# Kernel tuning notes

Hardware: AMD Instinct MI355X
Metric: run time of the kernel (lower is better)

## Reference

```python
import jax, jax.numpy as jnp
import numpy as np

NUM_HEADS = 16
ROPE_THETA = 10000.0


def _rope_cos_sin(seq_len, head_dim, dtype):
    # theta_i = theta^(-2i/d_k), i in [0, d_k/2)
    i = jnp.arange(head_dim // 2, dtype=jnp.float32)
    inv_freq = ROPE_THETA ** (-2.0 * i / head_dim)
    pos = jnp.arange(seq_len, dtype=jnp.float32)[:, None]
    ang = pos * inv_freq[None, :]                      # [S, d/2]
    return jnp.cos(ang).astype(dtype), jnp.sin(ang).astype(dtype)


def _apply_rope(t, cos, sin):
    # t: [B, H, S, d]; rotate consecutive pairs (complex multiply)
    B, H, S, d = t.shape
    tp = t.reshape(B, H, S, d // 2, 2)
    x0, x1 = tp[..., 0], tp[..., 1]
    r0 = x0 * cos - x1 * sin
    r1 = x0 * sin + x1 * cos
    return jnp.stack([r0, r1], axis=-1).reshape(B, H, S, d)


def setup_inputs() -> dict:
    key = jax.random.key(0)
    k1, k2, k3 = jax.random.split(key, 3)
    B, S, D = 4, 2048, 1024
    x = jax.random.normal(k1, (B, S, D), dtype=jnp.float32)
    padding_mask = jnp.ones((B, S), dtype=jnp.int32)
    # trunc-normal-ish init, std = sqrt(2/(in+out))
    std_qkv = np.sqrt(2.0 / (D + 3 * D))
    w_qkv = jax.random.normal(k2, (3 * D, D), dtype=jnp.float32) * std_qkv
    w_o = jax.random.normal(k3, (D, D), dtype=jnp.float32) * 0.02
    return {"x": x, "padding_mask": padding_mask, "w_qkv": w_qkv, "w_o": w_o}


def reference(x, padding_mask, w_qkv, w_o):
    B, S, D = x.shape
    H = NUM_HEADS
    hd = D // H
    scale = 1.0 / np.sqrt(hd)

    qkv = x @ w_qkv.T                                   # [B, S, 3D]
    q, k, v = jnp.split(qkv, 3, axis=-1)

    def to_heads(t):
        return t.reshape(B, S, H, hd).transpose(0, 2, 1, 3)  # [B, H, S, hd]

    q, k, v = to_heads(q), to_heads(k), to_heads(v)

    cos, sin = _rope_cos_sin(S, hd, x.dtype)            # [S, hd/2]
    q = _apply_rope(q, cos, sin)
    k = _apply_rope(k, cos, sin)

    scores = jnp.einsum("bhqd,bhkd->bhqk", q, k) * scale  # [B, H, S, S]

    causal = jnp.tril(jnp.ones((S, S), dtype=x.dtype))
    mask = causal[None, :, :] * padding_mask.astype(x.dtype)[:, None, :]  # [B, S, S]
    scores = jnp.where(mask[:, None, :, :] == 0, -jnp.inf, scores)

    weights = jax.nn.softmax(scores, axis=-1)
    out = jnp.einsum("bhqk,bhkd->bhqd", weights, v)     # [B, H, S, hd]
    out = out.transpose(0, 2, 1, 3).reshape(B, S, D)
    return out @ w_o.T
```

## Files before the change

kernel.cpp:

```cpp
#include <hip/hip_runtime.h>

typedef unsigned short u16;
typedef unsigned int u32;
typedef __bf16 bf16x8 __attribute__((ext_vector_type(8)));
typedef float f32x4 __attribute__((ext_vector_type(4)));

#define MFMA_BF16(a, b, c) __builtin_amdgcn_mfma_f32_16x16x32_bf16((a), (b), (c), 0, 0, 0)

#define QSCALE 0.18033688011112042f
#define M0SHIFT 24.0f


__device__ __forceinline__ u16 f2bf(float f) {
  u32 u = __builtin_bit_cast(u32, f);
  u += 0x7fffu + ((u >> 16) & 1u);
  return (u16)(u >> 16);
}

__device__ __forceinline__ void async_copy16(const void* g, void* l) {
  __builtin_amdgcn_global_load_lds(
      (__attribute__((address_space(1))) void*)g,
      (__attribute__((address_space(3))) void*)l, 16, 0, 0);
}


__global__ __launch_bounds__(256) void prep_kernel(
    const float* __restrict__ x_f, const float* __restrict__ wqkv_f,
    const float* __restrict__ wo_f, u16* __restrict__ xb,
    u16* __restrict__ wqkvb, u16* __restrict__ wob, float2* __restrict__ rope_t) {
  const int blk = blockIdx.x;
  if (blk < 12288) {
    const float* src;
    u16* dst;
    int base;
    float scale = 1.0f;
    if (blk < 8192)      { src = x_f;    dst = xb;    base = blk; }
    else if (blk < 11264){ src = wqkv_f; dst = wqkvb; base = blk - 8192;
                           if (base < 1024) scale = QSCALE; }
    else                 { src = wo_f;   dst = wob;   base = blk - 11264; }
    const int i = base * 1024 + threadIdx.x * 4;
    const float4 v = *(const float4*)(src + i);
    ushort4 o;
    o.x = f2bf(v.x * scale); o.y = f2bf(v.y * scale);
    o.z = f2bf(v.z * scale); o.w = f2bf(v.w * scale);
    *(ushort4*)(dst + i) = o;
  } else {
    const int idx = (blk - 12288) * 256 + threadIdx.x;
    const int s = idx >> 5, i = idx & 31;
    const float invf = __builtin_amdgcn_exp2f(-(float)i * 0.41524101186092027f);
    float rev = (float)s * invf * 0.15915494309189535f;
    rev -= floorf(rev);
    rope_t[idx] = make_float2(__builtin_amdgcn_cosf(rev), __builtin_amdgcn_sinf(rev));
  }
}


__device__ __forceinline__ void gemm_bt_tile(const u16* A, const u16* B, int K,
                                             int row0, int col0,
                                             u16* lds, f32x4 acc[4][4]) {
  const int tid = threadIdx.x;
  const int wave = tid >> 6;
  const int lane = tid & 63;
  const int fr = lane & 15;
  const int quad = lane >> 4;
  const int wm = (wave >> 1) * 64;
  const int wn = (wave & 1) * 64;
  u16* a_lds = lds;
  u16* b_lds = lds + 4096;

  f32x4 zero = {0.f, 0.f, 0.f, 0.f};
#pragma unroll
  for (int mt = 0; mt < 4; ++mt)
#pragma unroll
    for (int nt = 0; nt < 4; ++nt) acc[mt][nt] = zero;

  for (int k0 = 0; k0 < K; k0 += 32) {
    __syncthreads();
#pragma unroll
    for (int c = 0; c < 2; ++c) {
      const int ebase = wave * 1024 + c * 512;
      const int e = ebase + lane * 8;
      const int r = e >> 5;
      const int kk = e & 31;
      async_copy16(A + (size_t)(row0 + r) * K + k0 + kk, a_lds + ebase);
      async_copy16(B + (size_t)(col0 + r) * K + k0 + kk, b_lds + ebase);
    }
    __syncthreads();

    bf16x8 a_frag[4], b_frag[4];
#pragma unroll
    for (int t = 0; t < 4; ++t) {
      a_frag[t] = *(const bf16x8*)(a_lds + (wm + t * 16 + fr) * 32 + quad * 8);
      b_frag[t] = *(const bf16x8*)(b_lds + (wn + t * 16 + fr) * 32 + quad * 8);
    }
#pragma unroll
    for (int mt = 0; mt < 4; ++mt)
#pragma unroll
      for (int nt = 0; nt < 4; ++nt)
        acc[mt][nt] = MFMA_BF16(a_frag[mt], b_frag[nt], acc[mt][nt]);
  }
}


__global__ __launch_bounds__(256) void qkv_rope_kernel(
    const u16* __restrict__ x, const u16* __restrict__ w_qkv,
    const float2* __restrict__ rope_t,
    u16* __restrict__ q_ws, u16* __restrict__ k_ws, u16* __restrict__ vt_ws) {
  __shared__ u16 sbuf[128 * 136];
  f32x4 acc[4][4];
  const int row0 = blockIdx.y * 128;
  const int col0 = blockIdx.x * 128;
  gemm_bt_tile(x, w_qkv, 1024, row0, col0, sbuf, acc);

  const int tid = threadIdx.x;
  const int wave = tid >> 6, lane = tid & 63;
  const int fr = lane & 15, quad = lane >> 4;
  const int wm = (wave >> 1) * 64, wn = (wave & 1) * 64;
  const int region = col0 >> 10;
  const int f0 = col0 & 1023;
  const int s0r = row0 & 2047;
  const int bb = row0 >> 11;

  __syncthreads();

  if (region < 2) {
#pragma unroll
    for (int mt = 0; mt < 4; ++mt) {
#pragma unroll
      for (int nt = 0; nt < 4; ++nt) {
        const int n = wn + nt * 16 + fr;
        const int d = n & 63;
#pragma unroll
        for (int r = 0; r < 4; ++r) {
          const int m = wm + mt * 16 + quad * 4 + r;
          const float own = acc[mt][nt][r];
          const float part = __shfl_xor(own, 1);
          const int s = s0r + m;
          const float2 cssn = rope_t[s * 32 + (d >> 1)];
          const float val = (d & 1) ? (part * cssn.y + own * cssn.x)
                                    : (own * cssn.x - part * cssn.y);
          sbuf[m * 136 + n] = f2bf(val);
        }
      }
    }
    __syncthreads();
    u16* dst = (region == 0) ? q_ws : k_ws;
    const int h0 = f0 >> 6;
#pragma unroll
    for (int j = 0; j < 8; ++j) {
      const int idx2 = j * 256 + tid;
      const int hf = idx2 >> 10;
      const int m = (idx2 & 1023) >> 3;
      const int c8 = (idx2 & 7) * 8;
      const uint4 v = *(const uint4*)(sbuf + m * 136 + hf * 64 + c8);
      *(uint4*)(dst + ((size_t)(bb * 16 + h0 + hf) * 2048 + s0r + m) * 64 + c8) = v;
    }
  } else {
#pragma unroll
    for (int mt = 0; mt < 4; ++mt)
#pragma unroll
      for (int nt = 0; nt < 4; ++nt) {
        const int n = wn + nt * 16 + fr;
#pragma unroll
        for (int r = 0; r < 4; ++r) {
          const int m = wm + mt * 16 + quad * 4 + r;
          sbuf[n * 136 + m] = f2bf(acc[mt][nt][r]);
        }
      }
    __syncthreads();
    const int h0 = f0 >> 6;
#pragma unroll
    for (int j = 0; j < 8; ++j) {
      const int idx2 = j * 256 + tid;
      const int n = idx2 >> 4;
      const int mc = (idx2 & 15) * 8;
      const int h = h0 + (n >> 6);
      const int d = n & 63;
      const uint4 v = *(const uint4*)(sbuf + n * 136 + mc);
      *(uint4*)(vt_ws + ((size_t)(bb * 16 + h) * 64 + d) * 2048 + s0r + mc) = v;
    }
  }
}


__global__ __launch_bounds__(256, 3) void flash_attn_kernel(
    const u16* __restrict__ Q, const u16* __restrict__ K, const u16* __restrict__ Vt,
    const int* __restrict__ pad, u16* __restrict__ O) {
  const int S = 2048;
  const int idx = blockIdx.x;
  const int bh = idx & 63;
  const int b = bh >> 4, h = bh & 15;
  const int j = (idx >> 6) & 3;
  const int sr = idx >> 8;
  const int qt_rev = (sr >> 1) * 8 + ((sr & 1) ? (7 - j) : j);
  const int q0 = (15 - qt_rev) * 128;
  const u16* Qh = Q + (size_t)bh * S * 64;
  const u16* Kh = K + (size_t)bh * S * 64;
  const u16* Vth = Vt + (size_t)bh * 64 * S;
  const int tid = threadIdx.x, wave = tid >> 6, lane = tid & 63;
  const int fr = lane & 15, quad = lane >> 4;

  __shared__ u16 lds_k[2][2 * 64 * 32];
  __shared__ u16 lds_vt[2][2 * 64 * 32];
  __shared__ u16 lds_p[4][32 * 76];
  __shared__ float lds_bias[2][64];

  const int qb = q0 + wave * 32;
  bf16x8 qfrag[2][2];
#pragma unroll
  for (int mt = 0; mt < 2; ++mt)
#pragma unroll
    for (int kk = 0; kk < 2; ++kk)
      qfrag[mt][kk] =
          *(const bf16x8*)(Qh + (size_t)(qb + mt * 16 + fr) * 64 + kk * 32 + quad * 8);

  bf16x8 ones;
#pragma unroll
  for (int jj = 0; jj < 8; ++jj) ones[jj] = (__bf16)1.0f;

  f32x4 zero = {0.f, 0.f, 0.f, 0.f};
  f32x4 o_acc[2][4], lacc[2];
#pragma unroll
  for (int mt = 0; mt < 2; ++mt) {
    lacc[mt] = zero;
#pragma unroll
    for (int nt = 0; nt < 4; ++nt) o_acc[mt][nt] = zero;
  }

  u16* pw = lds_p[wave];
  const float NEG = -__builtin_inff();

  auto stage = [&](int k0, int bufi) {
#pragma unroll
    for (int it = 0; it < 2; ++it) {
      const int slot = it * 256 + tid;
      const int row = tid >> 2;
      const int c8 = (tid & 3) * 8;
      async_copy16(Kh + (size_t)(k0 + row) * 64 + it * 32 + c8,
                   &lds_k[bufi][slot * 8]);
      async_copy16(Vth + (size_t)row * 2048 + k0 + it * 32 + c8,
                   &lds_vt[bufi][slot * 8]);
    }
    if (tid < 64) lds_bias[bufi][tid] = pad[b * S + k0 + tid] ? -M0SHIFT : NEG;
  };

  const int kend = q0 + 64;
  stage(0, 0);
  __syncthreads();
  int cur = 0;

  for (int k0 = 0; k0 <= kend; k0 += 64) {
    if (k0 < kend) stage(k0 + 64, cur ^ 1);

    if (k0 <= qb + 31) {
      const u16* lk = lds_k[cur];
      const u16* lvt = lds_vt[cur];
      const float* lb = lds_bias[cur];
      const bool needMask = (k0 + 63 > qb);
#pragma unroll
      for (int nt = 0; nt < 4; ++nt) {
        f32x4 s0 = zero, s1 = zero;
#pragma unroll
        for (int kk = 0; kk < 2; ++kk) {
          bf16x8 bfrag =
              *(const bf16x8*)(lk + (kk * 64 + nt * 16 + fr) * 32 + quad * 8);
          s0 = MFMA_BF16(qfrag[0][kk], bfrag, s0);
          s1 = MFMA_BF16(qfrag[1][kk], bfrag, s1);
        }
        const float bias = lb[nt * 16 + fr];
        const int col = k0 + nt * 16 + fr;
#pragma unroll
        for (int r = 0; r < 4; ++r) {
          float v0 = s0[r] + bias;
          float v1 = s1[r] + bias;
          if (needMask) {
            if (col > qb + quad * 4 + r) v0 = NEG;
            if (col > qb + 16 + quad * 4 + r) v1 = NEG;
          }
          const float p0 = __builtin_amdgcn_exp2f(v0);
          const float p1 = __builtin_amdgcn_exp2f(v1);
          pw[(quad * 4 + r) * 76 + nt * 16 + fr] =
              (u16)(__builtin_bit_cast(u32, p0) >> 16);
          pw[(16 + quad * 4 + r) * 76 + nt * 16 + fr] =
              (u16)(__builtin_bit_cast(u32, p1) >> 16);
        }
      }
      asm volatile("s_waitcnt lgkmcnt(0)" ::: "memory");

#pragma unroll
      for (int kk = 0; kk < 2; ++kk) {
        bf16x8 p0 = *(const bf16x8*)(pw + fr * 76 + kk * 32 + quad * 8);
        bf16x8 p1 = *(const bf16x8*)(pw + (16 + fr) * 76 + kk * 32 + quad * 8);
        lacc[0] = MFMA_BF16(p0, ones, lacc[0]);
        lacc[1] = MFMA_BF16(p1, ones, lacc[1]);
#pragma unroll
        for (int nt = 0; nt < 4; ++nt) {
          bf16x8 vf =
              *(const bf16x8*)(lvt + (kk * 64 + nt * 16 + fr) * 32 + quad * 8);
          o_acc[0][nt] = MFMA_BF16(p0, vf, o_acc[0][nt]);
          o_acc[1][nt] = MFMA_BF16(p1, vf, o_acc[1][nt]);
        }
      }
    }

    __syncthreads();
    cur ^= 1;
  }

#pragma unroll
  for (int mt = 0; mt < 2; ++mt)
#pragma unroll
    for (int r = 0; r < 4; ++r) {
      const int row = qb + mt * 16 + quad * 4 + r;
      const float l = lacc[mt][r];
      const float rl = (l > 0.f) ? (1.0f / l) : 0.f;
#pragma unroll
      for (int nt = 0; nt < 4; ++nt)
        O[(size_t)(b * S + row) * 1024 + h * 64 + nt * 16 + fr] =
            f2bf(o_acc[mt][nt][r] * rl);
    }
}


__global__ __launch_bounds__(256) void oproj_kernel(
    const u16* __restrict__ A, const u16* __restrict__ w_o, float* __restrict__ out) {
  __shared__ u16 lds[8192];
  f32x4 acc[4][4];
  const int row0 = blockIdx.y * 128;
  const int col0 = blockIdx.x * 128;
  gemm_bt_tile(A, w_o, 1024, row0, col0, lds, acc);
  const int tid = threadIdx.x;
  const int wave = tid >> 6, lane = tid & 63;
  const int fr = lane & 15, quad = lane >> 4;
  const int wm = (wave >> 1) * 64, wn = (wave & 1) * 64;
#pragma unroll
  for (int mt = 0; mt < 4; ++mt)
#pragma unroll
    for (int nt = 0; nt < 4; ++nt) {
      const int ncol = col0 + wn + nt * 16 + fr;
#pragma unroll
      for (int r = 0; r < 4; ++r) {
        const int mrow = row0 + wm + mt * 16 + quad * 4 + r;
        out[(size_t)mrow * 1024 + ncol] = acc[mt][nt][r];
      }
    }
}


extern "C" void kernel_launch(void* const* d_in, const int* in_sizes, int n_in,
                              void* d_out, int out_size, void* d_ws, size_t ws_size,
                              hipStream_t stream) {
  const float* x_f = (const float*)d_in[0];
  const int* pad = (const int*)d_in[1];
  const float* wqkv_f = (const float*)d_in[2];
  const float* wo_f = (const float*)d_in[3];
  float* out = (float*)d_out;

  const int NX = 4 * 2048 * 1024;
  const int NWQKV = 3072 * 1024;
  const int NWO = 1024 * 1024;
  const size_t HSZ = (size_t)4 * 16 * 2048 * 64;

  u16* xb = (u16*)d_ws;
  u16* wqkvb = xb + NX;
  u16* wob = wqkvb + NWQKV;
  u16* q_ws = wob + NWO;
  u16* k_ws = q_ws + HSZ;
  u16* vt_ws = k_ws + HSZ;
  u16* attn_ws = vt_ws + HSZ;
  float2* rope_t = (float2*)(attn_ws + HSZ);

  dim3 blk(256);
  prep_kernel<<<dim3(12544), blk, 0, stream>>>(x_f, wqkv_f, wo_f, xb, wqkvb, wob, rope_t);
  qkv_rope_kernel<<<dim3(24, 64), blk, 0, stream>>>(xb, wqkvb, rope_t, q_ws, k_ws, vt_ws);
  flash_attn_kernel<<<dim3(1024), blk, 0, stream>>>(q_ws, k_ws, vt_ws, pad, attn_ws);
  oproj_kernel<<<dim3(8, 64), blk, 0, stream>>>(attn_ws, wob, out);
}
```

Baseline: 289.2 us.

## Rewrite projection GEMMs as 256x128 double-buffered tiles with swizzled LDS

Replaces the 128x128 single-buffer GEMM tile (K step 32, two syncthreads per step) with a 512-thread 256x128 tile using K step 64. Global-to-LDS async copies are double-buffered, the LDS layout is XOR-swizzled to avoid bank conflicts, and the MFMA phases are interleaved with barriers and priority hints. This targets load latency and LDS stalls in the QKV and output projection GEMMs. The cost is larger LDS per block, fewer blocks on the grid, and a hardcoded K=1024.

```diff
diff --git a/kernel.cpp b/kernel.cpp
--- a/kernel.cpp
+++ b/kernel.cpp
@@ -9,6 +9,14 @@
 
 #define QSCALE 0.18033688011112042f
 #define M0SHIFT 24.0f
+
+#define BARRIER __builtin_amdgcn_s_barrier()
+#define LGKM0                                                \
+  do {                                                       \
+    asm volatile("s_waitcnt lgkmcnt(0)" ::: "memory");       \
+    __builtin_amdgcn_sched_barrier(0);                       \
+  } while (0)
+#define WAIT_VM(N) asm volatile("s_waitcnt vmcnt(" #N ")" ::: "memory")
 
 
 __device__ __forceinline__ u16 f2bf(float f) {
@@ -55,18 +63,22 @@
 }
 
 
-__device__ __forceinline__ void gemm_bt_tile(const u16* A, const u16* B, int K,
-                                             int row0, int col0,
-                                             u16* lds, f32x4 acc[4][4]) {
+__device__ __forceinline__ void gemm256_bt(const u16* __restrict__ A,
+                                           const u16* __restrict__ B,
+                                           int row0, int col0, u16* lds,
+                                           f32x4 acc[4][4]) {
   const int tid = threadIdx.x;
-  const int wave = tid >> 6;
-  const int lane = tid & 63;
-  const int fr = lane & 15;
-  const int quad = lane >> 4;
+  const int wave = tid >> 6, lane = tid & 63;
+  const int fr = lane & 15, quad = lane >> 4;
   const int wm = (wave >> 1) * 64;
   const int wn = (wave & 1) * 64;
-  u16* a_lds = lds;
-  u16* b_lds = lds + 4096;
+  u16* bufA0 = lds;
+  u16* bufB0 = lds + 16384;
+  u16* bufA1 = lds + 24576;
+  u16* bufB1 = lds + 40960;
+
+  const int l8 = lane >> 3, l7 = lane & 7;
+  const int csw = (l7 ^ l8) * 8;
 
   f32x4 zero = {0.f, 0.f, 0.f, 0.f};
 #pragma unroll
@@ -74,43 +86,127 @@
 #pragma unroll
     for (int nt = 0; nt < 4; ++nt) acc[mt][nt] = zero;
 
-  for (int k0 = 0; k0 < K; k0 += 32) {
-    __syncthreads();
+  auto stage = [&](int t) {
+    u16* ba = (t & 1) ? bufA1 : bufA0;
+    u16* bb = (t & 1) ? bufB1 : bufB0;
+    const int k0 = t * 64;
+#pragma unroll
+    for (int c = 0; c < 4; ++c) {
+      const int ch = c * 8 + wave;
+      async_copy16(A + (size_t)(row0 + ch * 8 + l8) * 1024 + k0 + csw,
+                   ba + ch * 512);
+    }
 #pragma unroll
     for (int c = 0; c < 2; ++c) {
-      const int ebase = wave * 1024 + c * 512;
-      const int e = ebase + lane * 8;
-      const int r = e >> 5;
-      const int kk = e & 31;
-      async_copy16(A + (size_t)(row0 + r) * K + k0 + kk, a_lds + ebase);
-      async_copy16(B + (size_t)(col0 + r) * K + k0 + kk, b_lds + ebase);
-    }
-    __syncthreads();
-
-    bf16x8 a_frag[4], b_frag[4];
-#pragma unroll
-    for (int t = 0; t < 4; ++t) {
-      a_frag[t] = *(const bf16x8*)(a_lds + (wm + t * 16 + fr) * 32 + quad * 8);
-      b_frag[t] = *(const bf16x8*)(b_lds + (wn + t * 16 + fr) * 32 + quad * 8);
-    }
-#pragma unroll
-    for (int mt = 0; mt < 4; ++mt)
-#pragma unroll
-      for (int nt = 0; nt < 4; ++nt)
-        acc[mt][nt] = MFMA_BF16(a_frag[mt], b_frag[nt], acc[mt][nt]);
+      const int ch = c * 8 + wave;
+      async_copy16(B + (size_t)(col0 + ch * 8 + l8) * 1024 + k0 + csw,
+                   bb + ch * 512);
+    }
+  };
+
+  const int f7 = fr & 7;
+  const int sw0 = (quad ^ f7) * 8;
+  const int sw1 = ((quad + 4) ^ f7) * 8;
+  const int ar0 = (wm + fr) * 64, ar1 = (wm + 16 + fr) * 64;
+  const int ar2 = (wm + 32 + fr) * 64, ar3 = (wm + 48 + fr) * 64;
+  const int br0 = (wn + fr) * 64, br1 = (wn + 16 + fr) * 64;
+  const int br2 = (wn + 32 + fr) * 64, br3 = (wn + 48 + fr) * 64;
+
+  stage(0);
+  stage(1);
+  WAIT_VM(6);
+  BARRIER;
+
+  for (int t = 0; t < 16; ++t) {
+    const u16* ba = (t & 1) ? bufA1 : bufA0;
+    const u16* bb = (t & 1) ? bufB1 : bufB0;
+
+    bf16x8 a0k0 = *(const bf16x8*)(ba + ar0 + sw0);
+    bf16x8 a0k1 = *(const bf16x8*)(ba + ar0 + sw1);
+    bf16x8 a1k0 = *(const bf16x8*)(ba + ar1 + sw0);
+    bf16x8 a1k1 = *(const bf16x8*)(ba + ar1 + sw1);
+    bf16x8 b0k0 = *(const bf16x8*)(bb + br0 + sw0);
+    bf16x8 b0k1 = *(const bf16x8*)(bb + br0 + sw1);
+    bf16x8 b1k0 = *(const bf16x8*)(bb + br1 + sw0);
+    bf16x8 b1k1 = *(const bf16x8*)(bb + br1 + sw1);
+    BARRIER;
+    LGKM0;
+    __builtin_amdgcn_s_setprio(1);
+    acc[0][0] = MFMA_BF16(a0k0, b0k0, acc[0][0]);
+    acc[0][1] = MFMA_BF16(a0k0, b1k0, acc[0][1]);
+    acc[1][0] = MFMA_BF16(a1k0, b0k0, acc[1][0]);
+    acc[1][1] = MFMA_BF16(a1k0, b1k0, acc[1][1]);
+    acc[0][0] = MFMA_BF16(a0k1, b0k1, acc[0][0]);
+    acc[0][1] = MFMA_BF16(a0k1, b1k1, acc[0][1]);
+    acc[1][0] = MFMA_BF16(a1k1, b0k1, acc[1][0]);
+    acc[1][1] = MFMA_BF16(a1k1, b1k1, acc[1][1]);
+    __builtin_amdgcn_s_setprio(0);
+    BARRIER;
+
+    bf16x8 b2k0 = *(const bf16x8*)(bb + br2 + sw0);
+    bf16x8 b2k1 = *(const bf16x8*)(bb + br2 + sw1);
+    bf16x8 b3k0 = *(const bf16x8*)(bb + br3 + sw0);
+    bf16x8 b3k1 = *(const bf16x8*)(bb + br3 + sw1);
+    BARRIER;
+    LGKM0;
+    __builtin_amdgcn_s_setprio(1);
+    acc[0][2] = MFMA_BF16(a0k0, b2k0, acc[0][2]);
+    acc[0][3] = MFMA_BF16(a0k0, b3k0, acc[0][3]);
+    acc[1][2] = MFMA_BF16(a1k0, b2k0, acc[1][2]);
+    acc[1][3] = MFMA_BF16(a1k0, b3k0, acc[1][3]);
+    acc[0][2] = MFMA_BF16(a0k1, b2k1, acc[0][2]);
+    acc[0][3] = MFMA_BF16(a0k1, b3k1, acc[0][3]);
+    acc[1][2] = MFMA_BF16(a1k1, b2k1, acc[1][2]);
+    acc[1][3] = MFMA_BF16(a1k1, b3k1, acc[1][3]);
+    __builtin_amdgcn_s_setprio(0);
+    BARRIER;
+
+    bf16x8 a2k0 = *(const bf16x8*)(ba + ar2 + sw0);
+    bf16x8 a2k1 = *(const bf16x8*)(ba + ar2 + sw1);
+    bf16x8 a3k0 = *(const bf16x8*)(ba + ar3 + sw0);
+    bf16x8 a3k1 = *(const bf16x8*)(ba + ar3 + sw1);
+    BARRIER;
+    LGKM0;
+    __builtin_amdgcn_s_setprio(1);
+    acc[2][0] = MFMA_BF16(a2k0, b0k0, acc[2][0]);
+    acc[2][1] = MFMA_BF16(a2k0, b1k0, acc[2][1]);
+    acc[3][0] = MFMA_BF16(a3k0, b0k0, acc[3][0]);
+    acc[3][1] = MFMA_BF16(a3k0, b1k0, acc[3][1]);
+    acc[2][0] = MFMA_BF16(a2k1, b0k1, acc[2][0]);
+    acc[2][1] = MFMA_BF16(a2k1, b1k1, acc[2][1]);
+    acc[3][0] = MFMA_BF16(a3k1, b0k1, acc[3][0]);
+    acc[3][1] = MFMA_BF16(a3k1, b1k1, acc[3][1]);
+    acc[2][2] = MFMA_BF16(a2k0, b2k0, acc[2][2]);
+    acc[2][3] = MFMA_BF16(a2k0, b3k0, acc[2][3]);
+    acc[3][2] = MFMA_BF16(a3k0, b2k0, acc[3][2]);
+    acc[3][3] = MFMA_BF16(a3k0, b3k0, acc[3][3]);
+    acc[2][2] = MFMA_BF16(a2k1, b2k1, acc[2][2]);
+    acc[2][3] = MFMA_BF16(a2k1, b3k1, acc[2][3]);
+    acc[3][2] = MFMA_BF16(a3k1, b2k1, acc[3][2]);
+    acc[3][3] = MFMA_BF16(a3k1, b3k1, acc[3][3]);
+    __builtin_amdgcn_s_setprio(0);
+
+    BARRIER;
+    if (t + 2 < 16) {
+      stage(t + 2);
+      WAIT_VM(6);
+    } else if (t + 2 == 16) {
+      WAIT_VM(0);
+    }
+    BARRIER;
   }
 }
 
 
-__global__ __launch_bounds__(256) void qkv_rope_kernel(
+__global__ __launch_bounds__(512, 2) void qkv_rope_kernel(
     const u16* __restrict__ x, const u16* __restrict__ w_qkv,
     const float2* __restrict__ rope_t,
     u16* __restrict__ q_ws, u16* __restrict__ k_ws, u16* __restrict__ vt_ws) {
-  __shared__ u16 sbuf[128 * 136];
+  __shared__ u16 lds[49152];
   f32x4 acc[4][4];
-  const int row0 = blockIdx.y * 128;
+  const int row0 = blockIdx.y * 256;
   const int col0 = blockIdx.x * 128;
-  gemm_bt_tile(x, w_qkv, 1024, row0, col0, sbuf, acc);
+  gemm256_bt(x, w_qkv, row0, col0, lds, acc);
 
   const int tid = threadIdx.x;
   const int wave = tid >> 6, lane = tid & 63;
@@ -120,8 +216,8 @@
   const int f0 = col0 & 1023;
   const int s0r = row0 & 2047;
   const int bb = row0 >> 11;
-
-  __syncthreads();
+  const int h0 = f0 >> 6;
+
 
   if (region < 2) {
 #pragma unroll
@@ -139,20 +235,20 @@
           const float2 cssn = rope_t[s * 32 + (d >> 1)];
           const float val = (d & 1) ? (part * cssn.y + own * cssn.x)
                                     : (own * cssn.x - part * cssn.y);
-          sbuf[m * 136 + n] = f2bf(val);
+          lds[m * 136 + n] = f2bf(val);
         }
       }
     }
     __syncthreads();
     u16* dst = (region == 0) ? q_ws : k_ws;
-    const int h0 = f0 >> 6;
 #pragma unroll
     for (int j = 0; j < 8; ++j) {
-      const int idx2 = j * 256 + tid;
-      const int hf = idx2 >> 10;
-      const int m = (idx2 & 1023) >> 3;
-      const int c8 = (idx2 & 7) * 8;
-      const uint4 v = *(const uint4*)(sbuf + m * 136 + hf * 64 + c8);
+      const int idx2 = j * 512 + tid;
+      const int m = idx2 >> 4;
+      const int rem = idx2 & 15;
+      const int hf = rem >> 3;
+      const int c8 = (rem & 7) * 8;
+      const uint4 v = *(const uint4*)(lds + m * 136 + hf * 64 + c8);
       *(uint4*)(dst + ((size_t)(bb * 16 + h0 + hf) * 2048 + s0r + m) * 64 + c8) = v;
     }
   } else {
@@ -164,19 +260,18 @@
 #pragma unroll
         for (int r = 0; r < 4; ++r) {
           const int m = wm + mt * 16 + quad * 4 + r;
-          sbuf[n * 136 + m] = f2bf(acc[mt][nt][r]);
+          lds[n * 264 + m] = f2bf(acc[mt][nt][r]);
         }
       }
     __syncthreads();
-    const int h0 = f0 >> 6;
 #pragma unroll
     for (int j = 0; j < 8; ++j) {
-      const int idx2 = j * 256 + tid;
-      const int n = idx2 >> 4;
-      const int mc = (idx2 & 15) * 8;
+      const int idx2 = j * 512 + tid;
+      const int n = idx2 >> 5;
+      const int mc = (idx2 & 31) * 8;
       const int h = h0 + (n >> 6);
       const int d = n & 63;
-      const uint4 v = *(const uint4*)(sbuf + n * 136 + mc);
+      const uint4 v = *(const uint4*)(lds + n * 264 + mc);
       *(uint4*)(vt_ws + ((size_t)(bb * 16 + h) * 64 + d) * 2048 + s0r + mc) = v;
     }
   }
@@ -322,13 +417,13 @@
 }
 
 
-__global__ __launch_bounds__(256) void oproj_kernel(
+__global__ __launch_bounds__(512, 2) void oproj_kernel(
     const u16* __restrict__ A, const u16* __restrict__ w_o, float* __restrict__ out) {
-  __shared__ u16 lds[8192];
+  __shared__ u16 lds[49152];
   f32x4 acc[4][4];
-  const int row0 = blockIdx.y * 128;
+  const int row0 = blockIdx.y * 256;
   const int col0 = blockIdx.x * 128;
-  gemm_bt_tile(A, w_o, 1024, row0, col0, lds, acc);
+  gemm256_bt(A, w_o, row0, col0, lds, acc);
   const int tid = threadIdx.x;
   const int wave = tid >> 6, lane = tid & 63;
   const int fr = lane & 15, quad = lane >> 4;
@@ -370,9 +465,11 @@
   u16* attn_ws = vt_ws + HSZ;
   float2* rope_t = (float2*)(attn_ws + HSZ);
 
-  dim3 blk(256);
-  prep_kernel<<<dim3(12544), blk, 0, stream>>>(x_f, wqkv_f, wo_f, xb, wqkvb, wob, rope_t);
-  qkv_rope_kernel<<<dim3(24, 64), blk, 0, stream>>>(xb, wqkvb, rope_t, q_ws, k_ws, vt_ws);
-  flash_attn_kernel<<<dim3(1024), blk, 0, stream>>>(q_ws, k_ws, vt_ws, pad, attn_ws);
-  oproj_kernel<<<dim3(8, 64), blk, 0, stream>>>(attn_ws, wob, out);
-}
+  prep_kernel<<<dim3(12544), dim3(256), 0, stream>>>(x_f, wqkv_f, wo_f, xb, wqkvb,
+                                                     wob, rope_t);
+  qkv_rope_kernel<<<dim3(24, 32), dim3(512), 0, stream>>>(xb, wqkvb, rope_t, q_ws,
+                                                          k_ws, vt_ws);
+  flash_attn_kernel<<<dim3(1024), dim3(256), 0, stream>>>(q_ws, k_ws, vt_ws, pad,
+                                                          attn_ws);
+  oproj_kernel<<<dim3(8, 32), dim3(512), 0, stream>>>(attn_ws, wob, out);
+}
```

Result: faster. 276.8 us (-4.3%).
